# Optimization experiments

Measured on AMD Instinct MI355X. Metric: run time of the kernel, lower is better.

Reference implementation:

```python
import jax, jax.numpy as jnp
import numpy as np

NORM_CONST = 11.0  # from __init__ norm_const


def _to_blocks(x, s):
    # [B,C,T,H,W] -> [B,C,T,H//s,W//s,s*s]
    B, C, T, H, W = x.shape
    hg, wg = H // s, W // s
    xb = x.reshape(B, C, T, hg, s, wg, s)
    xb = jnp.transpose(xb, (0, 1, 2, 3, 5, 4, 6))
    return xb.reshape(B, C, T, hg, wg, s * s)


def _from_blocks(q, s, H, W):
    # [B,C,T,hg,wg,s*s] -> [B,C,T,H,W]
    B, C, T, hg, wg, _ = q.shape
    qb = q.reshape(B, C, T, hg, wg, s, s)
    qb = jnp.transpose(qb, (0, 1, 2, 3, 5, 4, 6))
    return qb.reshape(B, C, T, H, W)


def setup_inputs() -> dict:
    key = jax.random.key(0)
    k1, k2 = jax.random.split(key)
    shape = (4, 1, 12, 800, 800)
    pred = jax.random.uniform(k1, shape, dtype=jnp.float32)
    inp = jax.random.uniform(k2, shape, dtype=jnp.float32)
    return {"pred_log_norm": pred, "input_mosaic_log_norm": inp, "scale": 10}


def reference(pred_log_norm, input_mosaic_log_norm, scale):
    s = int(scale)
    B, C, T, H, W = pred_log_norm.shape
    n = s * s

    # to linear domain, non-negative
    pred_lin = jnp.clip(jnp.expm1(pred_log_norm * NORM_CONST), 0.0)
    inp_lin = jnp.clip(jnp.expm1(input_mosaic_log_norm * NORM_CONST), 0.0)

    p_blocks = _to_blocks(pred_lin, s)            # [B,C,T,hg,wg,n]
    # avg_pool3d(1,s,s) * n == block sum
    S = _to_blocks(inp_lin, s).sum(axis=-1)       # [B,C,T,hg,wg]

    # water-filling (simplex-style) projection per block
    u = -jnp.sort(-p_blocks, axis=-1)             # descending sort
    cssv = jnp.cumsum(u, axis=-1)
    k = jnp.arange(1, n + 1, dtype=p_blocks.dtype)
    t = (cssv - S[..., None]) / k
    mask = u > t
    rho = jnp.maximum(mask.sum(axis=-1, keepdims=True), 1)  # clamp(min=1)
    theta = jnp.take_along_axis(t, rho - 1, axis=-1)
    q = jnp.clip(p_blocks - theta, 0.0)

    corrected = _from_blocks(q, s, H, W)
    return jnp.log1p(corrected) / NORM_CONST
```

## Files before the change

kernel.cpp:

```cpp
#include <hip/hip_runtime.h>
#include <math.h>


constexpr float kNorm    = 11.0f;
constexpr float kInvNorm = 1.0f / 11.0f;

__global__ __launch_bounds__(256) void pcl_waterfill2_kernel(
    const float* __restrict__ pred,
    const float* __restrict__ inp,
    float* __restrict__ out,
    int n_blocks_total)
{
    const int tid  = blockIdx.x * 256 + threadIdx.x;
    const int wid  = tid >> 6;
    const int lane = tid & 63;
    const int half = lane >> 5;
    const int l32  = lane & 31;

    const int blk = wid * 2 + half;
    if (blk >= n_blocks_total) return;

    const int img = blk / 6400;
    const int rem = blk - img * 6400;
    const int by  = rem / 80;
    const int bx  = rem - by * 80;

    const float* predI = pred + (long long)img * 640000LL;
    const float* inpI  = inp  + (long long)img * 640000LL;
    float*       outI  = out  + (long long)img * 640000LL;

    const int rowBase = by * 10;
    const int colBase = bx * 10;

    float p[4];
    int   addr[4];
    float sloc = 0.0f;
    float ploc = 0.0f;
    #pragma unroll
    for (int k = 0; k < 4; ++k) {
        const int e = l32 + 32 * k;
        if (e < 100) {
            const int r = e / 10;
            const int c = e - r * 10;
            const int a = (rowBase + r) * 800 + colBase + c;
            addr[k] = a;
            const float xp = predI[a];
            const float xi = inpI[a];
            const float pl = fmaxf(__expf(xp * kNorm) - 1.0f, 0.0f);
            const float sl = fmaxf(__expf(xi * kNorm) - 1.0f, 0.0f);
            p[k] = pl;
            ploc += pl;
            sloc += sl;
        } else {
            addr[k] = -1;
            p[k] = -INFINITY;
        }
    }

    float S = sloc, sumP = ploc;
    #pragma unroll
    for (int off = 16; off; off >>= 1) {
        S    += __shfl_xor(S, off);
        sumP += __shfl_xor(sumP, off);
    }

    float theta = (sumP - S) * 0.01f;
    float prevc = 100.0f;
    #pragma unroll 1
    for (int it = 0; it < 100; ++it) {
        float sm = 0.0f;
        unsigned long long bm0, bm1, bm2, bm3;
        {
            const bool a0 = (p[0] > theta); bm0 = __ballot(a0); if (a0) sm += p[0];
            const bool a1 = (p[1] > theta); bm1 = __ballot(a1); if (a1) sm += p[1];
            const bool a2 = (p[2] > theta); bm2 = __ballot(a2); if (a2) sm += p[2];
            const bool a3 = (p[3] > theta); bm3 = __ballot(a3); if (a3) sm += p[3];
        }
        #pragma unroll
        for (int off = 16; off; off >>= 1) sm += __shfl_xor(sm, off);

        const int cl = __popcll(bm0 & 0xffffffffull) + __popcll(bm1 & 0xffffffffull)
                     + __popcll(bm2 & 0xffffffffull) + __popcll(bm3 & 0xffffffffull);
        const int ch = __popcll(bm0 >> 32) + __popcll(bm1 >> 32)
                     + __popcll(bm2 >> 32) + __popcll(bm3 >> 32);
        const float fc = (half == 0) ? (float)cl : (float)ch;

        const bool stable = (fc == prevc) || (fc == 0.0f);
        if (!stable) theta = __fdividef(sm - S, fc);
        prevc = fc;
        if (__all(stable)) break;
    }

    #pragma unroll
    for (int k = 0; k < 4; ++k) {
        if (addr[k] >= 0) {
            const float q = fmaxf(p[k] - theta, 0.0f);
            outI[addr[k]] = __logf(1.0f + q) * kInvNorm;
        }
    }
}

extern "C" void kernel_launch(void* const* d_in, const int* in_sizes, int n_in,
                              void* d_out, int out_size, void* d_ws, size_t ws_size,
                              hipStream_t stream) {
    const float* pred = (const float*)d_in[0];
    const float* inp  = (const float*)d_in[1];
    float* out        = (float*)d_out;

    const int n_images = in_sizes[0] / (800 * 800);
    const int n_blocks = n_images * 6400;
    const int waves    = (n_blocks + 1) / 2;
    const int wgs      = (waves + 3) / 4;

    pcl_waterfill2_kernel<<<wgs, 256, 0, stream>>>(pred, inp, out, n_blocks);
}
```

Baseline: 94.46 us.

## Seed water-filling threshold from per-block LDS histogram of suffix sums

Each 100-element block is bucketed into 32 bins by its log-domain value using LDS atomics. A suffix scan over the bins then yields a starting threshold close to the final one, so fewer fixed-point iterations should be needed. The loop also zeroes out excluded elements, and the arithmetic moves to the exp domain, with the -1 offsets folded into S and tau. The cost is extra LDS atomics and a scan per block on a mostly memory-bound kernel.

Result: slower. 221.8 us (+134.8%).

```diff
diff --git a/kernel.cpp b/kernel.cpp
--- a/kernel.cpp
+++ b/kernel.cpp
@@ -5,97 +5,115 @@
 constexpr float kNorm    = 11.0f;
 constexpr float kInvNorm = 1.0f / 11.0f;
 
-__global__ __launch_bounds__(256) void pcl_waterfill2_kernel(
+__global__ __launch_bounds__(256) void pcl_bucket_kernel(
     const float* __restrict__ pred,
     const float* __restrict__ inp,
     float* __restrict__ out,
     int n_blocks_total)
 {
-    const int tid  = blockIdx.x * 256 + threadIdx.x;
-    const int wid  = tid >> 6;
-    const int lane = tid & 63;
-    const int half = lane >> 5;
-    const int l32  = lane & 31;
+    __shared__ float binS[8][32];
+    __shared__ int   binC[8][32];
 
+    const int tx     = threadIdx.x;
+    const int region = tx >> 5;
+    const int l32    = tx & 31;
+    const int half   = region & 1;
+
+    const int wid = (blockIdx.x * 256 + tx) >> 6;
     const int blk = wid * 2 + half;
     if (blk >= n_blocks_total) return;
 
-    const int img = blk / 6400;
-    const int rem = blk - img * 6400;
-    const int by  = rem / 80;
-    const int bx  = rem - by * 80;
+    const int img  = blk / 6400;
+    const int rem  = blk - img * 6400;
+    const int by   = rem / 80;
+    const int bx   = rem - by * 80;
+    const int base = img * 640000 + by * 8000 + bx * 10;
 
-    const float* predI = pred + (long long)img * 640000LL;
-    const float* inpI  = inp  + (long long)img * 640000LL;
-    float*       outI  = out  + (long long)img * 640000LL;
-
-    const int rowBase = by * 10;
-    const int colBase = bx * 10;
+    binS[region][l32] = 0.0f;
+    binC[region][l32] = 0;
 
     float p[4];
     int   addr[4];
     float sloc = 0.0f;
-    float ploc = 0.0f;
     #pragma unroll
     for (int k = 0; k < 4; ++k) {
         const int e = l32 + 32 * k;
         if (e < 100) {
             const int r = e / 10;
             const int c = e - r * 10;
-            const int a = (rowBase + r) * 800 + colBase + c;
+            const int a = base + r * 800 + c;
             addr[k] = a;
-            const float xp = predI[a];
-            const float xi = inpI[a];
-            const float pl = fmaxf(__expf(xp * kNorm) - 1.0f, 0.0f);
-            const float sl = fmaxf(__expf(xi * kNorm) - 1.0f, 0.0f);
-            p[k] = pl;
-            ploc += pl;
-            sloc += sl;
+            const float xp = pred[a];
+            const float xi = inp[a];
+            float ep = fmaxf(__expf(xp * kNorm), 1.0f);
+            float ei = fmaxf(__expf(xi * kNorm), 1.0f);
+            p[k] = ep;
+            sloc += ei;
+            int j = (int)(xp * 32.0f);
+            j = j < 0 ? 0 : (j > 31 ? 31 : j);
+            atomicAdd(&binS[region][j], ep);
+            atomicAdd(&binC[region][j], 1);
         } else {
             addr[k] = -1;
-            p[k] = -INFINITY;
+            p[k] = 0.0f;
         }
     }
 
-    float S = sloc, sumP = ploc;
+    float S = sloc;
     #pragma unroll
-    for (int off = 16; off; off >>= 1) {
-        S    += __shfl_xor(S, off);
-        sumP += __shfl_xor(sumP, off);
+    for (int off = 16; off; off >>= 1) S += __shfl_xor(S, off);
+    S -= 100.0f;
+
+    float C  = binS[region][l32];
+    float Nf = (float)binC[region][l32];
+    #pragma unroll
+    for (int off = 1; off < 32; off <<= 1) {
+        const float tC = __shfl_down(C,  off, 32);
+        const float tN = __shfl_down(Nf, off, 32);
+        const bool ok = (l32 + off) < 32;
+        C  += ok ? tC : 0.0f;
+        Nf += ok ? tN : 0.0f;
     }
 
-    float theta = (sumP - S) * 0.01f;
-    float prevc = 100.0f;
+    float tau = (Nf > 0.5f) ? __fdividef(C - S, Nf) : -3.0e38f;
+    #pragma unroll
+    for (int off = 16; off; off >>= 1) tau = fmaxf(tau, __shfl_xor(tau, off));
+
+    float prevc = -1.0f;
     #pragma unroll 1
     for (int it = 0; it < 100; ++it) {
-        float sm = 0.0f;
-        unsigned long long bm0, bm1, bm2, bm3;
-        {
-            const bool a0 = (p[0] > theta); bm0 = __ballot(a0); if (a0) sm += p[0];
-            const bool a1 = (p[1] > theta); bm1 = __ballot(a1); if (a1) sm += p[1];
-            const bool a2 = (p[2] > theta); bm2 = __ballot(a2); if (a2) sm += p[2];
-            const bool a3 = (p[3] > theta); bm3 = __ballot(a3); if (a3) sm += p[3];
-        }
+        const bool a0 = p[0] > tau;
+        const bool a1 = p[1] > tau;
+        const bool a2 = p[2] > tau;
+        const bool a3 = p[3] > tau;
+        const unsigned long long b0 = __ballot(a0);
+        const unsigned long long b1 = __ballot(a1);
+        const unsigned long long b2 = __ballot(a2);
+        const unsigned long long b3 = __ballot(a3) & 0x0000000F0000000FULL;
+        p[0] = a0 ? p[0] : 0.0f;
+        p[1] = a1 ? p[1] : 0.0f;
+        p[2] = a2 ? p[2] : 0.0f;
+        p[3] = a3 ? p[3] : 0.0f;
+        float sm = (p[0] + p[1]) + (p[2] + p[3]);
         #pragma unroll
         for (int off = 16; off; off >>= 1) sm += __shfl_xor(sm, off);
-
-        const int cl = __popcll(bm0 & 0xffffffffull) + __popcll(bm1 & 0xffffffffull)
-                     + __popcll(bm2 & 0xffffffffull) + __popcll(bm3 & 0xffffffffull);
-        const int ch = __popcll(bm0 >> 32) + __popcll(bm1 >> 32)
-                     + __popcll(bm2 >> 32) + __popcll(bm3 >> 32);
-        const float fc = (half == 0) ? (float)cl : (float)ch;
-
-        const bool stable = (fc == prevc) || (fc == 0.0f);
-        if (!stable) theta = __fdividef(sm - S, fc);
+        const int cl = __popcll(b0 & 0xffffffffULL) + __popcll(b1 & 0xffffffffULL)
+                     + __popcll(b2 & 0xffffffffULL) + __popcll(b3 & 0xffffffffULL);
+        const int ch = __popcll(b0 >> 32) + __popcll(b1 >> 32)
+                     + __popcll(b2 >> 32) + __popcll(b3 >> 32);
+        const float fc = half ? (float)ch : (float)cl;
+        const bool stable = (fc == prevc) || (fc < 0.5f);
+        if (__all(stable)) break;
+        tau = stable ? tau : __fdividef(sm - S, fc);
         prevc = fc;
-        if (__all(stable)) break;
     }
 
+    const float tm1 = tau - 1.0f;
     #pragma unroll
     for (int k = 0; k < 4; ++k) {
         if (addr[k] >= 0) {
-            const float q = fmaxf(p[k] - theta, 0.0f);
-            outI[addr[k]] = __logf(1.0f + q) * kInvNorm;
+            const float q1 = fmaxf(p[k] - tm1, 1.0f);
+            out[addr[k]] = __logf(q1) * kInvNorm;
         }
     }
 }
@@ -112,5 +130,5 @@
     const int waves    = (n_blocks + 1) / 2;
     const int wgs      = (waves + 3) / 4;
 
-    pcl_waterfill2_kernel<<<wgs, 256, 0, stream>>>(pred, inp, out, n_blocks);
+    pcl_bucket_kernel<<<wgs, 256, 0, stream>>>(pred, inp, out, n_blocks);
 }
```
